# Performance work log

Measured on AMD Instinct MI355X. Metric: run time of the kernel, lower is better.

The kernel has to match this reference:

```python
import jax, jax.numpy as jnp
import numpy as np

N_VIS, N_HID, T, B = 784, 500, 256, 256


def setup_inputs() -> dict:
    key = jax.random.key(0)
    k_v, k_w, k_u = jax.random.split(key, 3)
    # binary spike-train style data, shape (n_visible, T, batch)
    v = (jax.random.uniform(k_v, (N_VIS, T, B)) < 0.5).astype(jnp.float32)
    W = 0.01 * jax.random.normal(k_w, (N_HID, N_VIS), dtype=jnp.float32)
    U = 0.01 * jax.random.normal(k_u, (N_HID, N_HID), dtype=jnp.float32)
    b_h = jnp.zeros((N_HID,), jnp.float32)
    b_v = jnp.zeros((N_VIS,), jnp.float32)
    b_init = jnp.zeros((N_HID,), jnp.float32)
    return {"v": v, "W": W, "U": U, "b_h": b_h, "b_v": b_v, "b_init": b_init}


def reference(v, W, U, b_h, b_v, b_init):
    """RTRBM.contrastive_divergence with CDk=1.

    v: (V, T, B). Returns (v_model, r_model) both time-major-in-middle like torch:
    v_model (V, T, B), r_model (H, T, B).
    """
    V, T_, B_ = v.shape
    H = W.shape[0]
    # t==0 uses b_init with no U @ r_lag term; emulate via r_lag0 = 0 and a
    # per-timestep hidden bias: b_init at t=0, b_h afterwards.
    bias_seq = jnp.concatenate(
        [b_init[None, :], jnp.broadcast_to(b_h, (T_ - 1, H))], axis=0)  # (T, H)
    keys = jax.random.split(jax.random.key(123), T_)
    v_seq = jnp.moveaxis(v, 1, 0)  # (T, V, B)

    def step(r_lag, xs):
        v_t, bias_t, k = xs                       # v_t: (V, B)
        pre = W @ v_t + U @ r_lag + bias_t[:, None]  # (H, B)
        r_data = jax.nn.sigmoid(pre)               # hidden means, carried as r_lag
        k1, k2 = jax.random.split(k)
        h_model = jax.random.bernoulli(k1, r_data).astype(v_t.dtype)
        v_mean = jax.nn.sigmoid(W.T @ h_model + b_v[:, None])  # (V, B)
        v_model = jax.random.bernoulli(k2, v_mean).astype(v_t.dtype)
        return r_data, (v_model, h_model)

    r0 = jnp.zeros((H, B_), v.dtype)
    _, (v_model, r_model) = jax.lax.scan(step, r0, (v_seq, bias_seq, keys))
    # back to torch layout: (V, T, B) and (H, T, B)
    return jnp.moveaxis(v_model, 0, 1), jnp.moveaxis(r_model, 0, 1)
```

## Files before the change

### kernel.cpp

```cpp
#include <hip/hip_runtime.h>
#include <stdint.h>

#define NV 784
#define NH 500
#define TT 256
#define BB 256
#define NBG 128

typedef float f2v __attribute__((ext_vector_type(2)));

__device__ __forceinline__ void tf2x32(uint32_t ks0, uint32_t ks1,
                                       uint32_t x0, uint32_t x1,
                                       uint32_t& y0, uint32_t& y1) {
  uint32_t ks2 = ks0 ^ ks1 ^ 0x1BD11BDAu;
  x0 += ks0; x1 += ks1;
#define TFROT(r) { x0 += x1; x1 = (x1 << (r)) | (x1 >> (32 - (r))); x1 ^= x0; }
  TFROT(13) TFROT(15) TFROT(26) TFROT(6)
  x0 += ks1; x1 += ks2 + 1u;
  TFROT(17) TFROT(29) TFROT(16) TFROT(24)
  x0 += ks2; x1 += ks0 + 2u;
  TFROT(13) TFROT(15) TFROT(26) TFROT(6)
  x0 += ks0; x1 += ks1 + 3u;
  TFROT(17) TFROT(29) TFROT(16) TFROT(24)
  x0 += ks1; x1 += ks2 + 4u;
  TFROT(13) TFROT(15) TFROT(26) TFROT(6)
  x0 += ks2; x1 += ks0 + 5u;
#undef TFROT
  y0 = x0; y1 = x1;
}

__device__ __forceinline__ float jax_uniform(uint32_t bits) {
#pragma clang fp contract(off)
  float f = __uint_as_float((bits >> 9) | 0x3F800000u);
  return f - 1.0f;
}

__device__ __forceinline__ uint32_t draw_bits(uint32_t k0, uint32_t k1,
                                              uint32_t j) {
  uint32_t y0, y1;
  tf2x32(k0, k1, 0u, j, y0, y1);
  return y0 ^ y1;
}

__device__ __forceinline__ float xla_expf(float x) {
#pragma clang fp contract(off)
  float xc = fminf(fmaxf(x, -88.3762626647949f), 88.3762626647950f);
  float fx = floorf(xc * 1.44269504088896341f + 0.5f);
  float tmp = 0.693359375f * fx;
  float z = -2.12194440e-4f * fx;
  float xr = xc - tmp;
  xr = xr - z;
  z = xr * xr;
  float y = xr * 1.9875691500e-4f + 1.3981999507e-3f;
  y = y * xr + 8.3334519073e-3f;
  y = y * xr + 4.1665795894e-2f;
  y = y * xr + 1.6666665459e-1f;
  y = y * xr + 5.0000001201e-1f;
  y = y * z + xr;
  y = 1.0f + y;
  int e = (int)fx;
  float pow2 = __int_as_float((uint32_t)(e + 127) << 23);
  return y * pow2;
}

__device__ __forceinline__ float xla_sigmoid(float x) {
#pragma clang fp contract(off)
  float e = xla_expf(-x);
  float d = 1.0f + e;
  return 1.0f / d;
}

__device__ __forceinline__ uint32_t extract_even(unsigned long long x) {
  x &= 0x5555555555555555ull;
  x = (x ^ (x >> 1)) & 0x3333333333333333ull;
  x = (x ^ (x >> 2)) & 0x0F0F0F0F0F0F0F0Full;
  x = (x ^ (x >> 4)) & 0x00FF00FF00FF00FFull;
  x = (x ^ (x >> 8)) & 0x0000FFFF0000FFFFull;
  x = (x ^ (x >> 16)) & 0x00000000FFFFFFFFull;
  return (uint32_t)x;
}

__global__ void init_keys(uint32_t* __restrict__ keys ) {
  int t = threadIdx.x;
  if (t >= TT) return;
  uint32_t kt0, kt1;
  tf2x32(0u, 123u, 0u, (uint32_t)t, kt0, kt1);
  uint32_t a0, a1, b0, b1;
  tf2x32(kt0, kt1, 0u, 0u, a0, a1);
  tf2x32(kt0, kt1, 0u, 1u, b0, b1);
  keys[4 * t + 0] = a0;
  keys[4 * t + 1] = a1;
  keys[4 * t + 2] = b0;
  keys[4 * t + 3] = b1;
}

__global__ __launch_bounds__(256) void wt_kernel(const float* __restrict__ W,
                                                 float* __restrict__ WT) {
  const int i = blockIdx.x;
  for (int k = threadIdx.x; k < NH; k += 256)
    WT[(size_t)i * NH + k] = W[(size_t)k * NV + i];
}

__global__ __launch_bounds__(512) void ut_kernel(const float* __restrict__ U,
                                                 float2* __restrict__ UTPC) {
  const int p = blockIdx.x;
  const int h = threadIdx.x;
  float2 w;
  if (h < NH) {
    w.x = U[(size_t)h * NH + 2 * p];
    w.y = U[(size_t)h * NH + 2 * p + 1];
  } else {
    w.x = 0.0f; w.y = 0.0f;
  }
  UTPC[((size_t)(p >> 3) * 512 + h) * 8 + (p & 7)] = w;
}

#define HT_A 20
__global__ __launch_bounds__(256, 4) void wv_gemm(
    const float* __restrict__ v, const float* __restrict__ W,
    float* __restrict__ wv2) {
#pragma clang fp contract(off)
  const int b = threadIdx.x;
  const int bid = (int)blockIdx.x;
  const int xcd = bid & 7;
  const int slot = bid >> 3;
  const int t = (slot / 25) * 8 + xcd;
  const int h0 = (slot % 25) * HT_A;
  const float* vcol = v + (size_t)t * BB + b;

  float acc[HT_A];
#pragma unroll
  for (int r = 0; r < HT_A; ++r) acc[r] = 0.0f;

  const int pb[4] = {0, 288, 576, 784};
#pragma unroll 1
  for (int p = 0; p < 3; ++p) {
    float ps[HT_A];
#pragma unroll
    for (int r = 0; r < HT_A; ++r) ps[r] = 0.0f;
    const int k0 = pb[p], k1 = pb[p + 1];
#pragma unroll 8
    for (int k = k0; k < k1; ++k) {
      float x = vcol[(size_t)k * (TT * BB)];
#pragma unroll
      for (int r = 0; r < HT_A; ++r)
        ps[r] = __builtin_fmaf(W[(size_t)(h0 + r) * NV + k], x, ps[r]);
    }
#pragma unroll
    for (int r = 0; r < HT_A; ++r) acc[r] = acc[r] + ps[r];
  }

  __shared__ float al[HT_A][BB + 1];
#pragma unroll
  for (int r = 0; r < HT_A; ++r) al[r][b] = acc[r];
  __syncthreads();

  const int sub = b / 40;
  const int idx = b % 40;
#pragma unroll 1
  for (int it = 0; it < 22; ++it) {
    const int bg = it * 6 + sub;
    if (b < 240 && bg < NBG) {
      wv2[((size_t)bg * TT + t) * 1024 + h0 * 2 + idx] =
          al[idx >> 1][2 * bg + (idx & 1)];
    }
  }
}

template <int CBASE, int NCHUNK, int REM>
__device__ __forceinline__ f2v dot_panel(const char* __restrict__ ubase,
                                         const float4* __restrict__ rq_cp) {
#pragma clang fp contract(off)
  float4 A0, A1, A2, A3, B0, B1, B2, B3, C0, C1, C2, C3;
  {
    const float4* s = (const float4*)(ubase + (size_t)CBASE * 32768);
    A0 = s[0]; A1 = s[1]; A2 = s[2]; A3 = s[3];
  }
  B0 = A0; B1 = A1; B2 = A2; B3 = A3;
  if (NCHUNK > 1) {
    const float4* s = (const float4*)(ubase + (size_t)(CBASE + 1) * 32768);
    B0 = s[0]; B1 = s[1]; B2 = s[2]; B3 = s[3];
  } else if (REM > 0) {
    const float4* s = (const float4*)(ubase + (size_t)(CBASE + 1) * 32768);
    B0 = s[0];
  }
  C0 = A0; C1 = A1; C2 = A2; C3 = A3;
  f2v acc; acc.x = 0.0f; acc.y = 0.0f;
#pragma unroll 1
  for (int c = 0; c < NCHUNK; ++c) {
    if (c + 2 < NCHUNK) {
      const float4* ns = (const float4*)(ubase + (size_t)(CBASE + c + 2) * 32768);
      C0 = ns[0]; C1 = ns[1]; C2 = ns[2]; C3 = ns[3];
    } else if (c + 2 == NCHUNK && REM > 0) {
      const float4* ns = (const float4*)(ubase + (size_t)(CBASE + c + 2) * 32768);
      C0 = ns[0];
    }
    const int pb = (CBASE + c) * 8;
#define PAIRSTEP(AR, S0, S1, i) { \
      const float4 r4 = rq_cp[2 * (pb + (i))]; \
      f2v ux; ux.x = AR.S0; ux.y = AR.S0; \
      f2v uy; uy.x = AR.S1; uy.y = AR.S1; \
      f2v r0; r0.x = r4.x; r0.y = r4.y; \
      f2v r1; r1.x = r4.z; r1.y = r4.w; \
      acc = acc + ux * r0; \
      acc = acc + uy * r1; }
    PAIRSTEP(A0, x, y, 0) PAIRSTEP(A0, z, w, 1)
    PAIRSTEP(A1, x, y, 2) PAIRSTEP(A1, z, w, 3)
    PAIRSTEP(A2, x, y, 4) PAIRSTEP(A2, z, w, 5)
    PAIRSTEP(A3, x, y, 6) PAIRSTEP(A3, z, w, 7)
#undef PAIRSTEP
    A0 = B0; A1 = B1; A2 = B2; A3 = B3;
    B0 = C0; B1 = C1; B2 = C2; B3 = C3;
  }
  if (REM > 0) {
    const int pb = (CBASE + NCHUNK) * 8;
    {
      const float4 r4 = rq_cp[2 * pb];
      f2v ux; ux.x = A0.x; ux.y = A0.x;
      f2v uy; uy.x = A0.y; uy.y = A0.y;
      f2v r0; r0.x = r4.x; r0.y = r4.y;
      f2v r1; r1.x = r4.z; r1.y = r4.w;
      acc = acc + ux * r0;
      acc = acc + uy * r1;
    }
    {
      const float4 r4 = rq_cp[2 * (pb + 1)];
      f2v ux; ux.x = A0.z; ux.y = A0.z;
      f2v uy; uy.x = A0.w; uy.y = A0.w;
      f2v r0; r0.x = r4.x; r0.y = r4.y;
      f2v r1; r1.x = r4.z; r1.y = r4.w;
      acc = acc + ux * r0;
      acc = acc + uy * r1;
    }
  }
  return acc;
}

__device__ __forceinline__ void poll_one(const uint32_t* __restrict__ prog,
                                         int p, uint32_t tgt, int tid) {
  for (;;) {
    uint32_t v = 0;
    if ((tid & 63) == 0)
      v = __hip_atomic_load(&prog[p * 32], __ATOMIC_RELAXED,
                            __HIP_MEMORY_SCOPE_AGENT);
    v = __builtin_amdgcn_readfirstlane(v);
    if (v >= tgt) break;
    __builtin_amdgcn_s_sleep(1);
  }
}

__device__ __forceinline__ void poll_two(const uint32_t* __restrict__ prog,
                                         int pa, int pb2, uint32_t tgt, int tid) {
  for (;;) {
    uint32_t va = 0, vb = 0;
    if ((tid & 63) == 0) {
      va = __hip_atomic_load(&prog[pa * 32], __ATOMIC_RELAXED,
                             __HIP_MEMORY_SCOPE_AGENT);
      vb = __hip_atomic_load(&prog[pb2 * 32], __ATOMIC_RELAXED,
                             __HIP_MEMORY_SCOPE_AGENT);
    }
    va = __builtin_amdgcn_readfirstlane(va);
    vb = __builtin_amdgcn_readfirstlane(vb);
    if (va >= tgt && vb >= tgt) break;
    __builtin_amdgcn_s_sleep(1);
  }
}

__global__ __launch_bounds__(512) void hidden_quad(
    const float2* __restrict__ UTPC, const float* __restrict__ b_h,
    const float* __restrict__ b_init, const uint32_t* __restrict__ keys,
    const float* __restrict__ wv2, uint32_t* __restrict__ hbw,
    unsigned long long* __restrict__ exch, uint32_t* __restrict__ prog) {
#pragma clang fp contract(off)
  const int tid = threadIdx.x;
  const int pan = tid >> 8;
  const int idx = tid & 255;
  const int cp = idx & 1;
  const int hl = idx >> 1;
  const int bid = (int)blockIdx.x;
  const int cg = bid & 63;
  const int q = bid >> 6;
  const int h = q * 128 + hl;
  const int hs = (h < NH) ? h : 0;
  const int bg = 2 * cg + cp;
  const int b0 = 2 * bg;

  __shared__ __align__(16) float4 rq[512];
  __shared__ f2v ps_l[256];
  __shared__ f2v u_l[256];
  __shared__ uint32_t keyl[2 * TT];

  keyl[tid] = keys[4 * (tid >> 1) + (tid & 1)];
  if (pan == 0) {
    float4 z; z.x = 0.0f; z.y = 0.0f; z.z = 0.0f; z.w = 0.0f;
    rq[idx] = z; rq[256 + idx] = z;
  }
  const float bh = b_h[hs], bi = b_init[hs];
  const char* __restrict__ ubase = (const char*)UTPC + (size_t)h * 64;
  f2v* __restrict__ rw = (f2v*)rq;
  const float4* __restrict__ rq_cp = rq + cp;
  const int p1 = (((q + 1) & 3) << 6) | cg;
  const int p2 = (((q + 2) & 3) << 6) | cg;
  const int p3 = (((q + 3) & 3) << 6) | cg;
  __syncthreads();

#pragma unroll 1
  for (int t = 0; t < TT; ++t) {
    f2v wvp; wvp.x = 0.0f; wvp.y = 0.0f;
    f2v a;
    if (pan == 0) {
      wvp = *(const f2v*)&wv2[((size_t)bg * TT + t) * 1024 + h * 2];
      a = dot_panel<0, 18, 0>(ubase, rq_cp);
    } else {
      a = dot_panel<18, 13, 2>(ubase, rq_cp);
      ps_l[hl * 2 + cp] = a;
      const uint32_t k0 = keyl[2 * t], k1 = keyl[2 * t + 1];
      f2v u;
      u.x = jax_uniform(draw_bits(k0, k1, (uint32_t)(h * BB + b0)));
      u.y = jax_uniform(draw_bits(k0, k1, (uint32_t)(h * BB + b0 + 1)));
      u_l[hl * 2 + cp] = u;
    }
    __syncthreads();

    bool hm0 = false, hm1 = false;
    if (pan == 0) {
      const f2v ps = ps_l[hl * 2 + cp];
      const float acc0 = a.x + ps.x;
      const float acc1 = a.y + ps.y;
      const float bias = (t == 0) ? bi : bh;
      const float pre0 = (wvp.x + acc0) + bias;
      const float pre1 = (wvp.y + acc1) + bias;
      const float pp0 = xla_sigmoid(pre0);
      const float pp1 = xla_sigmoid(pre1);
      f2v pv; pv.x = pp0; pv.y = pp1;
      rw[(h >> 1) * 4 + cp * 2 + (h & 1)] = pv;
      if (t != TT - 1) {
        __hip_atomic_store(&exch[((size_t)bid * 2 + (t & 1)) * 256 + idx],
                           __builtin_bit_cast(unsigned long long, pv),
                           __ATOMIC_RELAXED, __HIP_MEMORY_SCOPE_AGENT);
      }
      const f2v u = u_l[hl * 2 + cp];
      hm0 = u.x < pp0;
      hm1 = u.y < pp1;
    }

    __syncthreads();
    const uint32_t tgt = (uint32_t)(t + 1);
    if (tid == 0 && t != TT - 1)
      __hip_atomic_store(&prog[bid * 32], tgt,
                         __ATOMIC_RELAXED, __HIP_MEMORY_SCOPE_AGENT);

    if (pan == 0) {
      const unsigned long long m0 = __ballot(hm0);
      const unsigned long long m1 = __ballot(hm1);
      const uint32_t e0 = extract_even(m0);
      const uint32_t o0 = extract_even(m0 >> 1);
      const uint32_t e1 = extract_even(m1);
      const uint32_t o1 = extract_even(m1 >> 1);
      if ((tid & 63) == 0) {
        uint4 w4; w4.x = e0; w4.y = e1; w4.z = o0; w4.w = o1;
        *(uint4*)&hbw[(size_t)(h >> 5) * (TT * BB) + (size_t)t * BB + 4 * cg] = w4;
      }
    }
    if (t == TT - 1) break;

    if (pan == 0) {
      poll_one(prog, p1, tgt, tid);
      unsigned long long w = __hip_atomic_load(
          &exch[((size_t)p1 * 2 + (t & 1)) * 256 + idx],
          __ATOMIC_RELAXED, __HIP_MEMORY_SCOPE_AGENT);
      const int hh = (((q + 1) & 3) * 128) + hl;
      rw[(hh >> 1) * 4 + cp * 2 + (hh & 1)] = __builtin_bit_cast(f2v, w);
    } else {
      poll_two(prog, p2, p3, tgt, tid);
      unsigned long long w2 = __hip_atomic_load(
          &exch[((size_t)p2 * 2 + (t & 1)) * 256 + idx],
          __ATOMIC_RELAXED, __HIP_MEMORY_SCOPE_AGENT);
      unsigned long long w3 = __hip_atomic_load(
          &exch[((size_t)p3 * 2 + (t & 1)) * 256 + idx],
          __ATOMIC_RELAXED, __HIP_MEMORY_SCOPE_AGENT);
      const int hh2 = (((q + 2) & 3) * 128) + hl;
      const int hh3 = (((q + 3) & 3) * 128) + hl;
      rw[(hh2 >> 1) * 4 + cp * 2 + (hh2 & 1)] = __builtin_bit_cast(f2v, w2);
      rw[(hh3 >> 1) * 4 + cp * 2 + (hh3 & 1)] = __builtin_bit_cast(f2v, w3);
    }
    __syncthreads();
  }
}

__global__ __launch_bounds__(256) void expand_r(
    const uint32_t* __restrict__ hbw, float* __restrict__ out_r) {
  const int h = blockIdx.x;
  const int b = threadIdx.x;
  const uint32_t sh = (uint32_t)(h & 31);
  const uint32_t* src = hbw + (size_t)(h >> 5) * (TT * BB);
  float* dst = out_r + (size_t)h * (TT * BB);
#pragma unroll 4
  for (int t = 0; t < TT; ++t) {
    uint32_t w = src[t * BB + b];
    dst[t * BB + b] = (float)((w >> sh) & 1u);
  }
}

#define IT_C 16
__global__ __launch_bounds__(256, 4) void visible_big(
    const float* __restrict__ WT, const float* __restrict__ b_v,
    const uint32_t* __restrict__ keys, const float* __restrict__ hplane,
    float* __restrict__ out_v) {
#pragma clang fp contract(off)
  const int b = threadIdx.x;
  const int bid = (int)blockIdx.x;
  const int xcd = bid & 7;
  const int slot = bid >> 3;
  const int t = (slot / 49) * 8 + xcd;
  const int i0 = (slot % 49) * IT_C;
  const float* hcol = hplane + (size_t)t * BB + b;

  float acc[IT_C];
#pragma unroll
  for (int r = 0; r < IT_C; ++r) acc[r] = 0.0f;

  const int pb[3] = {0, 288, 500};
#pragma unroll 1
  for (int p = 0; p < 2; ++p) {
    float ps[IT_C];
#pragma unroll
    for (int r = 0; r < IT_C; ++r) ps[r] = 0.0f;
    const int k0 = pb[p], k1 = pb[p + 1];
#pragma unroll 8
    for (int k = k0; k < k1; ++k) {
      float hh = hcol[(size_t)k * (TT * BB)];
#pragma unroll
      for (int r = 0; r < IT_C; ++r)
        ps[r] = __builtin_fmaf(WT[(size_t)(i0 + r) * NH + k], hh, ps[r]);
    }
#pragma unroll
    for (int r = 0; r < IT_C; ++r) acc[r] = acc[r] + ps[r];
  }

  const uint32_t key0 = keys[4 * t + 2], key1 = keys[4 * t + 3];
#pragma unroll
  for (int r = 0; r < IT_C; ++r) {
    const int i = i0 + r;
    float pre = acc[r] + b_v[i];
    float p = xla_sigmoid(pre);
    uint32_t j = (uint32_t)(i * BB + b);
    float u = jax_uniform(draw_bits(key0, key1, j));
    out_v[(size_t)i * (TT * BB) + (size_t)t * BB + b] = (u < p) ? 1.0f : 0.0f;
  }
}

extern "C" void kernel_launch(void* const* d_in, const int* in_sizes, int n_in,
                              void* d_out, int out_size, void* d_ws, size_t ws_size,
                              hipStream_t stream) {
  const float* v      = (const float*)d_in[0];
  const float* W      = (const float*)d_in[1];
  const float* U      = (const float*)d_in[2];
  const float* b_h    = (const float*)d_in[3];
  const float* b_v    = (const float*)d_in[4];
  const float* b_init = (const float*)d_in[5];

  float* out_v = (float*)d_out;
  float* out_r = out_v + (size_t)NV * TT * BB;

  float* wv2 = out_v;
  unsigned long long* exch =
      (unsigned long long*)(out_v + (size_t)NBG * TT * 1024);
  uint32_t* prog = (uint32_t*)(exch + (size_t)256 * 2 * 256);
  float2* UTPC = (float2*)out_r;

  float* WT = (float*)d_ws;
  uint32_t* keys = (uint32_t*)(WT + (size_t)NV * NH);
  uint32_t* hbw = keys + TT * 4;

  hipMemsetAsync(prog, 0, 256 * 32 * sizeof(uint32_t), stream);
  init_keys<<<1, 256, 0, stream>>>(keys);
  wt_kernel<<<NV, 256, 0, stream>>>(W, WT);
  ut_kernel<<<250, 512, 0, stream>>>(U, UTPC);

  wv_gemm<<<25 * TT, 256, 0, stream>>>(v, W, wv2);

  hidden_quad<<<256, 512, 0, stream>>>(UTPC, b_h, b_init, keys, wv2, hbw,
                                       exch, prog);

  expand_r<<<NH, 256, 0, stream>>>(hbw, out_r);

  visible_big<<<49 * TT, 256, 0, stream>>>(WT, b_v, keys, out_r, out_v);
}
```

Baseline: 4.262 ms.

## Repartition hidden recurrence into 8 hidden groups of 64 with 4 batch pairs per block

The persistent hidden-state kernel changes its decomposition from 4 hidden-unit groups of 128 times 64 batch groups to 8 groups of 64 times 32 batch groups, with each thread pair handling 4 columns. Each block now reads a narrower slice of U, so per-block U traffic and the dependent dot-product chain shrink, but every block must poll and gather r from 7 peers instead of 3. The bit-packing of sampled hidden states changes to 16-bit words via a new compress routine, and the progress flag store now uses release ordering. This trades cheaper per-step compute against more cross-block synchronization per timestep.

```diff
diff --git a/kernel.cpp b/kernel.cpp
--- a/kernel.cpp
+++ b/kernel.cpp
@@ -70,13 +70,12 @@
   return 1.0f / d;
 }
 
-__device__ __forceinline__ uint32_t extract_even(unsigned long long x) {
-  x &= 0x5555555555555555ull;
-  x = (x ^ (x >> 1)) & 0x3333333333333333ull;
-  x = (x ^ (x >> 2)) & 0x0F0F0F0F0F0F0F0Full;
-  x = (x ^ (x >> 4)) & 0x00FF00FF00FF00FFull;
-  x = (x ^ (x >> 8)) & 0x0000FFFF0000FFFFull;
-  x = (x ^ (x >> 16)) & 0x00000000FFFFFFFFull;
+__device__ __forceinline__ uint32_t compress4(unsigned long long x) {
+  x &= 0x1111111111111111ull;
+  x = (x | (x >> 3))  & 0x0303030303030303ull;
+  x = (x | (x >> 6))  & 0x000F000F000F000Full;
+  x = (x | (x >> 12)) & 0x000000FF000000FFull;
+  x = (x | (x >> 24)) & 0x000000000000FFFFull;
   return (uint32_t)x;
 }
 
@@ -197,7 +196,7 @@
     }
     const int pb = (CBASE + c) * 8;
 #define PAIRSTEP(AR, S0, S1, i) { \
-      const float4 r4 = rq_cp[2 * (pb + (i))]; \
+      const float4 r4 = rq_cp[4 * (pb + (i))]; \
       f2v ux; ux.x = AR.S0; ux.y = AR.S0; \
       f2v uy; uy.x = AR.S1; uy.y = AR.S1; \
       f2v r0; r0.x = r4.x; r0.y = r4.y; \
@@ -215,7 +214,7 @@
   if (REM > 0) {
     const int pb = (CBASE + NCHUNK) * 8;
     {
-      const float4 r4 = rq_cp[2 * pb];
+      const float4 r4 = rq_cp[4 * pb];
       f2v ux; ux.x = A0.x; ux.y = A0.x;
       f2v uy; uy.x = A0.y; uy.y = A0.y;
       f2v r0; r0.x = r4.x; r0.y = r4.y;
@@ -224,7 +223,7 @@
       acc = acc + uy * r1;
     }
     {
-      const float4 r4 = rq_cp[2 * (pb + 1)];
+      const float4 r4 = rq_cp[4 * (pb + 1)];
       f2v ux; ux.x = A0.z; ux.y = A0.z;
       f2v uy; uy.x = A0.w; uy.y = A0.w;
       f2v r0; r0.x = r4.x; r0.y = r4.y;
@@ -236,72 +235,66 @@
   return acc;
 }
 
-__device__ __forceinline__ void poll_one(const uint32_t* __restrict__ prog,
-                                         int p, uint32_t tgt, int tid) {
+__device__ __forceinline__ void poll_n(const uint32_t* __restrict__ prog,
+                                       const int* pb4, int n, uint32_t tgt,
+                                       int tid) {
   for (;;) {
-    uint32_t v = 0;
-    if ((tid & 63) == 0)
-      v = __hip_atomic_load(&prog[p * 32], __ATOMIC_RELAXED,
-                            __HIP_MEMORY_SCOPE_AGENT);
-    v = __builtin_amdgcn_readfirstlane(v);
-    if (v >= tgt) break;
+    uint32_t ok = 1u;
+    if ((tid & 63) == 0) {
+#pragma unroll
+      for (int i = 0; i < 4; ++i) {
+        if (i < n) {
+          uint32_t v = __hip_atomic_load(&prog[pb4[i] * 32], __ATOMIC_RELAXED,
+                                         __HIP_MEMORY_SCOPE_AGENT);
+          ok &= (v >= tgt) ? 1u : 0u;
+        }
+      }
+    }
+    ok = __builtin_amdgcn_readfirstlane(ok);
+    if (ok) break;
     __builtin_amdgcn_s_sleep(1);
   }
 }
 
-__device__ __forceinline__ void poll_two(const uint32_t* __restrict__ prog,
-                                         int pa, int pb2, uint32_t tgt, int tid) {
-  for (;;) {
-    uint32_t va = 0, vb = 0;
-    if ((tid & 63) == 0) {
-      va = __hip_atomic_load(&prog[pa * 32], __ATOMIC_RELAXED,
-                             __HIP_MEMORY_SCOPE_AGENT);
-      vb = __hip_atomic_load(&prog[pb2 * 32], __ATOMIC_RELAXED,
-                             __HIP_MEMORY_SCOPE_AGENT);
-    }
-    va = __builtin_amdgcn_readfirstlane(va);
-    vb = __builtin_amdgcn_readfirstlane(vb);
-    if (va >= tgt && vb >= tgt) break;
-    __builtin_amdgcn_s_sleep(1);
-  }
-}
-
-__global__ __launch_bounds__(512) void hidden_quad(
+__global__ __launch_bounds__(512) void hidden_oct(
     const float2* __restrict__ UTPC, const float* __restrict__ b_h,
     const float* __restrict__ b_init, const uint32_t* __restrict__ keys,
-    const float* __restrict__ wv2, uint32_t* __restrict__ hbw,
+    const float* __restrict__ wv2, uint16_t* __restrict__ hb16,
     unsigned long long* __restrict__ exch, uint32_t* __restrict__ prog) {
 #pragma clang fp contract(off)
   const int tid = threadIdx.x;
   const int pan = tid >> 8;
   const int idx = tid & 255;
-  const int cp = idx & 1;
-  const int hl = idx >> 1;
+  const int cp = idx & 3;
+  const int hl = idx >> 2;
   const int bid = (int)blockIdx.x;
-  const int cg = bid & 63;
-  const int q = bid >> 6;
-  const int h = q * 128 + hl;
+  const int cg = bid & 31;
+  const int oct = bid >> 5;
+  const int h = oct * 64 + hl;
   const int hs = (h < NH) ? h : 0;
-  const int bg = 2 * cg + cp;
+  const int bg = 4 * cg + cp;
   const int b0 = 2 * bg;
 
-  __shared__ __align__(16) float4 rq[512];
+  __shared__ __align__(16) float4 rq[1024];
   __shared__ f2v ps_l[256];
   __shared__ f2v u_l[256];
   __shared__ uint32_t keyl[2 * TT];
 
   keyl[tid] = keys[4 * (tid >> 1) + (tid & 1)];
-  if (pan == 0) {
+  {
     float4 z; z.x = 0.0f; z.y = 0.0f; z.z = 0.0f; z.w = 0.0f;
-    rq[idx] = z; rq[256 + idx] = z;
+    rq[tid] = z; rq[512 + tid] = z;
   }
   const float bh = b_h[hs], bi = b_init[hs];
   const char* __restrict__ ubase = (const char*)UTPC + (size_t)h * 64;
   f2v* __restrict__ rw = (f2v*)rq;
   const float4* __restrict__ rq_cp = rq + cp;
-  const int p1 = (((q + 1) & 3) << 6) | cg;
-  const int p2 = (((q + 2) & 3) << 6) | cg;
-  const int p3 = (((q + 3) & 3) << 6) | cg;
+  int pb4[4];
+  const int pbase = pan ? 4 : 1;
+  const int pcnt = pan ? 4 : 3;
+#pragma unroll
+  for (int i = 0; i < 4; ++i)
+    pb4[i] = (((oct + pbase + i) & 7) << 5) | cg;
   __syncthreads();
 
 #pragma unroll 1
@@ -313,18 +306,18 @@
       a = dot_panel<0, 18, 0>(ubase, rq_cp);
     } else {
       a = dot_panel<18, 13, 2>(ubase, rq_cp);
-      ps_l[hl * 2 + cp] = a;
+      ps_l[hl * 4 + cp] = a;
       const uint32_t k0 = keyl[2 * t], k1 = keyl[2 * t + 1];
       f2v u;
       u.x = jax_uniform(draw_bits(k0, k1, (uint32_t)(h * BB + b0)));
       u.y = jax_uniform(draw_bits(k0, k1, (uint32_t)(h * BB + b0 + 1)));
-      u_l[hl * 2 + cp] = u;
+      u_l[hl * 4 + cp] = u;
     }
     __syncthreads();
 
     bool hm0 = false, hm1 = false;
     if (pan == 0) {
-      const f2v ps = ps_l[hl * 2 + cp];
+      const f2v ps = ps_l[hl * 4 + cp];
       const float acc0 = a.x + ps.x;
       const float acc1 = a.y + ps.y;
       const float bias = (t == 0) ? bi : bh;
@@ -333,13 +326,13 @@
       const float pp0 = xla_sigmoid(pre0);
       const float pp1 = xla_sigmoid(pre1);
       f2v pv; pv.x = pp0; pv.y = pp1;
-      rw[(h >> 1) * 4 + cp * 2 + (h & 1)] = pv;
+      rw[(h >> 1) * 8 + cp * 2 + (h & 1)] = pv;
       if (t != TT - 1) {
         __hip_atomic_store(&exch[((size_t)bid * 2 + (t & 1)) * 256 + idx],
                            __builtin_bit_cast(unsigned long long, pv),
                            __ATOMIC_RELAXED, __HIP_MEMORY_SCOPE_AGENT);
       }
-      const f2v u = u_l[hl * 2 + cp];
+      const f2v u = u_l[hl * 4 + cp];
       hm0 = u.x < pp0;
       hm1 = u.y < pp1;
     }
@@ -348,52 +341,44 @@
     const uint32_t tgt = (uint32_t)(t + 1);
     if (tid == 0 && t != TT - 1)
       __hip_atomic_store(&prog[bid * 32], tgt,
-                         __ATOMIC_RELAXED, __HIP_MEMORY_SCOPE_AGENT);
+                         __ATOMIC_RELEASE, __HIP_MEMORY_SCOPE_AGENT);
 
     if (pan == 0) {
       const unsigned long long m0 = __ballot(hm0);
       const unsigned long long m1 = __ballot(hm1);
-      const uint32_t e0 = extract_even(m0);
-      const uint32_t o0 = extract_even(m0 >> 1);
-      const uint32_t e1 = extract_even(m1);
-      const uint32_t o1 = extract_even(m1 >> 1);
-      if ((tid & 63) == 0) {
-        uint4 w4; w4.x = e0; w4.y = e1; w4.z = o0; w4.w = o1;
-        *(uint4*)&hbw[(size_t)(h >> 5) * (TT * BB) + (size_t)t * BB + 4 * cg] = w4;
+      const int l = tid & 63;
+      if (l < 8) {
+        const int cpe = l >> 1, je = l & 1;
+        const uint32_t bits16 = compress4((je ? m1 : m0) >> cpe);
+        const int h16 = oct * 4 + ((tid >> 6) & 3);
+        hb16[(size_t)h16 * (TT * BB) + (size_t)t * BB + 8 * cg + l] =
+            (uint16_t)bits16;
       }
     }
     if (t == TT - 1) break;
 
-    if (pan == 0) {
-      poll_one(prog, p1, tgt, tid);
-      unsigned long long w = __hip_atomic_load(
-          &exch[((size_t)p1 * 2 + (t & 1)) * 256 + idx],
-          __ATOMIC_RELAXED, __HIP_MEMORY_SCOPE_AGENT);
-      const int hh = (((q + 1) & 3) * 128) + hl;
-      rw[(hh >> 1) * 4 + cp * 2 + (hh & 1)] = __builtin_bit_cast(f2v, w);
-    } else {
-      poll_two(prog, p2, p3, tgt, tid);
-      unsigned long long w2 = __hip_atomic_load(
-          &exch[((size_t)p2 * 2 + (t & 1)) * 256 + idx],
-          __ATOMIC_RELAXED, __HIP_MEMORY_SCOPE_AGENT);
-      unsigned long long w3 = __hip_atomic_load(
-          &exch[((size_t)p3 * 2 + (t & 1)) * 256 + idx],
-          __ATOMIC_RELAXED, __HIP_MEMORY_SCOPE_AGENT);
-      const int hh2 = (((q + 2) & 3) * 128) + hl;
-      const int hh3 = (((q + 3) & 3) * 128) + hl;
-      rw[(hh2 >> 1) * 4 + cp * 2 + (hh2 & 1)] = __builtin_bit_cast(f2v, w2);
-      rw[(hh3 >> 1) * 4 + cp * 2 + (hh3 & 1)] = __builtin_bit_cast(f2v, w3);
+    poll_n(prog, pb4, pcnt, tgt, tid);
+#pragma unroll
+    for (int i = 0; i < 4; ++i) {
+      if (i < pcnt) {
+        const int po = (oct + pbase + i) & 7;
+        unsigned long long w = __hip_atomic_load(
+            &exch[((size_t)pb4[i] * 2 + (t & 1)) * 256 + idx],
+            __ATOMIC_RELAXED, __HIP_MEMORY_SCOPE_AGENT);
+        const int hh = po * 64 + hl;
+        rw[(hh >> 1) * 8 + cp * 2 + (hh & 1)] = __builtin_bit_cast(f2v, w);
+      }
     }
     __syncthreads();
   }
 }
 
 __global__ __launch_bounds__(256) void expand_r(
-    const uint32_t* __restrict__ hbw, float* __restrict__ out_r) {
+    const uint16_t* __restrict__ hb16, float* __restrict__ out_r) {
   const int h = blockIdx.x;
   const int b = threadIdx.x;
-  const uint32_t sh = (uint32_t)(h & 31);
-  const uint32_t* src = hbw + (size_t)(h >> 5) * (TT * BB);
+  const uint32_t sh = (uint32_t)(h & 15);
+  const uint16_t* src = hb16 + (size_t)(h >> 4) * (TT * BB);
   float* dst = out_r + (size_t)h * (TT * BB);
 #pragma unroll 4
   for (int t = 0; t < TT; ++t) {
@@ -471,7 +456,7 @@
 
   float* WT = (float*)d_ws;
   uint32_t* keys = (uint32_t*)(WT + (size_t)NV * NH);
-  uint32_t* hbw = keys + TT * 4;
+  uint16_t* hb16 = (uint16_t*)(keys + TT * 4);
 
   hipMemsetAsync(prog, 0, 256 * 32 * sizeof(uint32_t), stream);
   init_keys<<<1, 256, 0, stream>>>(keys);
@@ -480,10 +465,10 @@
 
   wv_gemm<<<25 * TT, 256, 0, stream>>>(v, W, wv2);
 
-  hidden_quad<<<256, 512, 0, stream>>>(UTPC, b_h, b_init, keys, wv2, hbw,
-                                       exch, prog);
-
-  expand_r<<<NH, 256, 0, stream>>>(hbw, out_r);
+  hidden_oct<<<256, 512, 0, stream>>>(UTPC, b_h, b_init, keys, wv2, hb16,
+                                      exch, prog);
+
+  expand_r<<<NH, 256, 0, stream>>>(hb16, out_r);
 
   visible_big<<<49 * TT, 256, 0, stream>>>(WT, b_v, keys, out_r, out_v);
 }
```

Measured after the change: 5.002 ms. 17.4% more time.
